# Kernel tuning notes

Measured on AMD Instinct MI355X. Metric: run time of the kernel, lower is better.

## Reference

```python
import jax, jax.numpy as jnp
import numpy as np

EPS = 1e-08


def setup_inputs() -> dict:
    key = jax.random.key(0)
    kx, km = jax.random.split(key)
    B, T, D = 128, 4096, 64
    x = jax.random.normal(kx, (B, T, D), dtype=jnp.float32)
    mask = jax.random.randint(km, (B, T, D), 0, 2).astype(jnp.float32)
    return {"x": x, "mask": mask}


def reference(x, mask):
    B, T, D = x.shape
    dt = x.dtype

    # ---- temporal: lag-1 autocorrelation + linear trend ----
    autocorr = jnp.mean(x[:, :-1, :] * x[:, 1:, :], axis=(1, 2))[:, None]  # (B,1)
    t = jnp.arange(T, dtype=dt)
    t_c = t - t.mean()
    x_mean_t = x.mean(axis=2)                                   # (B,T)
    num = (t_c * (x_mean_t - x_mean_t.mean(axis=1, keepdims=True))).sum(axis=1, keepdims=True)
    trend = num / ((t_c ** 2).sum() + EPS)                      # (B,1)

    # ---- frequency: dominant frequency + spectral entropy ----
    power = jnp.abs(jnp.fft.rfft(x_mean_t, axis=1)) ** 2        # (B,T//2+1)
    dom_freq = (jnp.argmax(power, axis=1).astype(dt) / (T / 2))[:, None]
    p_norm = power / (power.sum(axis=1, keepdims=True) + EPS)
    spec_ent = -(p_norm * jnp.log(p_norm + EPS)).sum(axis=1, keepdims=True)

    # ---- statistical: skewness, kurtosis, quantiles ----
    xc = x - x.mean(axis=(1, 2), keepdims=True)
    m2 = (xc ** 2).mean(axis=(1, 2))
    m3 = (xc ** 3).mean(axis=(1, 2))
    m4 = (xc ** 4).mean(axis=(1, 2))
    skew = m3 / (m2 ** 1.5 + EPS)
    kurt = m4 / (m2 ** 2 + EPS)
    q = jnp.quantile(x.reshape(B, -1), jnp.array([0.25, 0.5, 0.75]), axis=1)  # (3,B)
    stat = jnp.stack([skew, kurt, q[0], q[1], q[2]], axis=1)    # (B,5)

    # ---- shape: peaks, zero crossings, rate of change ----
    diff = x_mean_t[:, 1:] - x_mean_t[:, :-1]                   # (B,T-1)
    peak = (diff[:, 1:] * diff[:, :-1] < 0).astype(dt).sum(axis=1, keepdims=True) / (T - 2)
    xmc = x_mean_t - x_mean_t.mean(axis=1, keepdims=True)
    zero_cross = (xmc[:, 1:] * xmc[:, :-1] < 0).astype(dt).sum(axis=1, keepdims=True) / (T - 1)
    roc = jnp.abs(diff).mean(axis=1, keepdims=True)

    # ---- missing-data features (vectorized, no per-batch loop) ----
    missing_rate = 1.0 - mask.reshape(B, -1).sum(axis=1, keepdims=True) / (T * D + EPS)
    obs_per_time = mask.sum(axis=2)                             # (B,T)
    obs_density = obs_per_time / (D + EPS)
    density_var = jnp.var(obs_density, axis=1, ddof=1, keepdims=True)  # unbiased, matches torch
    time_mask = obs_per_time > 0                                # (B,T) bool
    first_idx = jnp.argmax(time_mask, axis=1).astype(dt)
    first_obs = jnp.where(time_mask.any(axis=1), first_idx / T, 0.0)[:, None]

    # ---- channel features: mean off-diagonal correlation + PCA var explained ----
    xcc = x - x.mean(axis=1, keepdims=True)                     # (B,T,D)
    gram = jnp.einsum('btd,bte->bde', xcc, xcc)                 # (B,D,D)
    cov = gram / (T - 1 + EPS)
    std = jnp.std(x, axis=1, ddof=1)                            # (B,D), unbiased like torch.std
    corr = cov / (std[:, :, None] * std[:, None, :] + EPS)
    off_diag = 1.0 - jnp.eye(D, dtype=dt)
    mean_corr = ((corr * off_diag).sum(axis=(1, 2)) / (D * (D - 1) + EPS))[:, None]
    # singular values squared of xcc == eigenvalues of gram
    eig = jnp.linalg.eigvalsh(gram)                             # ascending, (B,D)
    var_explained = (eig[:, -1] / eig.sum(axis=1))[:, None]

    return jnp.concatenate([
        autocorr, trend,               # temporal (2)
        dom_freq, spec_ent,            # frequency (2)
        stat,                          # statistical (5)
        peak, zero_cross, roc,         # shape (3)
        missing_rate, density_var, first_obs,  # missing (3)
        mean_corr, var_explained,      # channel (2)
    ], axis=1)                          # (B,17)
```

## Files before the change

kernel.cpp:

```cpp
#include <hip/hip_runtime.h>
#include <math.h>

#define TB 128
#define TT 4096
#define TD 64

#define GRAM_OFF   0u
#define HIST_OFF   2097152u
#define COLSUM_OFF 4194304u
#define SCAL_OFF   4227072u
#define FIRST_OFF  4230656u
#define ZERO_BYTES 4231168u
#define XMEAN_OFF  4231168u

typedef float  f32x4  __attribute__((ext_vector_type(4)));
typedef short  s16x8  __attribute__((ext_vector_type(8)));

__device__ __forceinline__ float brs4(float v, float* sbuf, int tid) {
#pragma unroll
  for (int o = 32; o; o >>= 1) v += __shfl_xor(v, o);
  __syncthreads();
  if ((tid & 63) == 0) sbuf[tid >> 6] = v;
  __syncthreads();
  return (sbuf[0] + sbuf[1]) + (sbuf[2] + sbuf[3]);
}

__device__ __forceinline__ float brs8(float v, float* sbuf, int tid) {
#pragma unroll
  for (int o = 32; o; o >>= 1) v += __shfl_xor(v, o);
  __syncthreads();
  if ((tid & 63) == 0) sbuf[tid >> 6] = v;
  __syncthreads();
  return ((sbuf[0] + sbuf[1]) + (sbuf[2] + sbuf[3])) +
         ((sbuf[4] + sbuf[5]) + (sbuf[6] + sbuf[7]));
}

__device__ __forceinline__ int binof(float v) {
  int bi = (int)floorf(fmaf(v, 256.f, 2048.f));
  return bi < 0 ? 0 : (bi > 4095 ? 4095 : bi);
}

__device__ __forceinline__ unsigned short f2bf(float f) {
  unsigned u = __float_as_uint(f);
  return (unsigned short)((u + 0x7FFFu + ((u >> 16) & 1u)) >> 16);
}

__global__ __launch_bounds__(256) void k1_fused(const float* __restrict__ x,
    const float* __restrict__ mk, float* __restrict__ xmean,
    float* __restrict__ gram, unsigned* __restrict__ hist,
    float* __restrict__ colsum, float* __restrict__ scal,
    int* __restrict__ firstg) {
  __shared__ __align__(16) float rows[64 * 72];
  __shared__ __align__(16) unsigned short Xt[64 * 72];
  __shared__ unsigned shist[4096];
  __shared__ float scol[64];
  __shared__ float sred[4];
  __shared__ int smax[4];

  const int tid  = threadIdx.x;
  const int b    = blockIdx.y;
  const int s    = blockIdx.x;
  const int t0   = s << 10;
  const int lane = tid & 63;
  const int wv   = tid >> 6;
  const int r0   = (tid >> 4) << 2;
  const int lcol = (tid & 15) << 2;
  const int rr   = tid >> 2;
  const int qq   = tid & 3;
  const int mb0 = (wv & 1) << 5;
  const int nb0 = (wv >> 1) << 5;
  const int ml  = lane & 15;
  const int qk  = (lane >> 4) << 3;

  for (int i = tid; i < 4096; i += 256) shist[i] = 0u;
  if (tid < 64) scol[tid] = 0.f;

  float s1 = 0.f, s2 = 0.f, s3 = 0.f, s4 = 0.f, ac = 0.f;
  float osum = 0.f, o2 = 0.f;
  int fmax = 0;
  float cs[4] = {0.f, 0.f, 0.f, 0.f};
  f32x4 acc[2][2];
#pragma unroll
  for (int mi = 0; mi < 2; ++mi)
#pragma unroll
    for (int ni = 0; ni < 2; ++ni) acc[mi][ni] = (f32x4)0.f;

  const float* xb = x + (size_t)b * (TT * TD);
  const float* mb = mk + (size_t)b * (TT * TD);

  __syncthreads();

  for (int tile = 0; tile < 16; ++tile) {
    const int tbase = t0 + (tile << 6);
    float4 v[4];
#pragma unroll
    for (int k = 0; k < 4; ++k) {
      const int r = r0 + k;
      v[k] = *(const float4*)(xb + (size_t)(tbase + r) * TD + lcol);
      const float x0 = v[k].x, x1 = v[k].y, x2 = v[k].z, x3 = v[k].w;
      const float q0 = x0 * x0, q1 = x1 * x1, q2 = x2 * x2, q3 = x3 * x3;
      s1 += (x0 + x1) + (x2 + x3);
      s2 += (q0 + q1) + (q2 + q3);
      s3 += (q0 * x0 + q1 * x1) + (q2 * x2 + q3 * x3);
      s4 += (q0 * q0 + q1 * q1) + (q2 * q2 + q3 * q3);
      cs[0] += x0; cs[1] += x1; cs[2] += x2; cs[3] += x3;
      atomicAdd(&shist[binof(x0)], 1u);
      atomicAdd(&shist[binof(x1)], 1u);
      atomicAdd(&shist[binof(x2)], 1u);
      atomicAdd(&shist[binof(x3)], 1u);
      *(float4*)(&rows[r * 72 + lcol]) = v[k];
    }
#pragma unroll
    for (int j = 0; j < 4; ++j) {
      const float e0 = j == 0 ? v[0].x : (j == 1 ? v[0].y : (j == 2 ? v[0].z : v[0].w));
      const float e1 = j == 0 ? v[1].x : (j == 1 ? v[1].y : (j == 2 ? v[1].z : v[1].w));
      const float e2 = j == 0 ? v[2].x : (j == 1 ? v[2].y : (j == 2 ? v[2].z : v[2].w));
      const float e3 = j == 0 ? v[3].x : (j == 1 ? v[3].y : (j == 2 ? v[3].z : v[3].w));
      uint2 pw;
      pw.x = (unsigned)f2bf(e0) | ((unsigned)f2bf(e1) << 16);
      pw.y = (unsigned)f2bf(e2) | ((unsigned)f2bf(e3) << 16);
      *(uint2*)(&Xt[(lcol + j) * 72 + r0]) = pw;
    }
#pragma unroll
    for (int k = 0; k < 4; ++k) {
      const int t = tbase + r0 + k;
      const float4 mv = *(const float4*)(mb + (size_t)t * TD + lcol);
      float ms = (mv.x + mv.y) + (mv.z + mv.w);
      ms += __shfl_xor(ms, 1);
      ms += __shfl_xor(ms, 2);
      ms += __shfl_xor(ms, 4);
      ms += __shfl_xor(ms, 8);
      if ((tid & 15) == 0) {
        osum += ms;
        o2 = fmaf(ms, ms, o2);
        if (ms > 0.f) fmax = max(fmax, TT - t);
      }
    }
    __syncthreads();
    {
      float4 c4[4];
      float rsum = 0.f;
#pragma unroll
      for (int j = 0; j < 4; ++j) {
        c4[j] = *(const float4*)(&rows[rr * 72 + (qq << 2) + (j << 4)]);
        rsum += (c4[j].x + c4[j].y) + (c4[j].z + c4[j].w);
      }
      float dot = 0.f;
      if (rr < 63) {
#pragma unroll
        for (int j = 0; j < 4; ++j) {
          const float4 n = *(const float4*)(&rows[(rr + 1) * 72 + (qq << 2) + (j << 4)]);
          dot += (c4[j].x * n.x + c4[j].y * n.y) + (c4[j].z * n.z + c4[j].w * n.w);
        }
      } else if (tbase + 64 < TT) {
        const float* np = xb + (size_t)(tbase + 64) * TD;
#pragma unroll
        for (int j = 0; j < 4; ++j) {
          const float4 n = *(const float4*)(np + (qq << 2) + (j << 4));
          dot += (c4[j].x * n.x + c4[j].y * n.y) + (c4[j].z * n.z + c4[j].w * n.w);
        }
      }
      ac += dot;
      rsum += __shfl_xor(rsum, 1);
      rsum += __shfl_xor(rsum, 2);
      if (qq == 0) xmean[(size_t)b * TT + tbase + rr] = rsum * (1.f / 64.f);
    }
#pragma unroll
    for (int kk = 0; kk < 2; ++kk) {
      const int ko = (kk << 5) + qk;
      s16x8 af[2], bf[2];
#pragma unroll
      for (int mi = 0; mi < 2; ++mi)
        af[mi] = *(const s16x8*)(&Xt[(mb0 + (mi << 4) + ml) * 72 + ko]);
#pragma unroll
      for (int ni = 0; ni < 2; ++ni)
        bf[ni] = *(const s16x8*)(&Xt[(nb0 + (ni << 4) + ml) * 72 + ko]);
#pragma unroll
      for (int mi = 0; mi < 2; ++mi)
#pragma unroll
        for (int ni = 0; ni < 2; ++ni)
          acc[mi][ni] = __builtin_amdgcn_mfma_f32_16x16x32_bf16(
              af[mi], bf[ni], acc[mi][ni], 0, 0, 0);
    }
    __syncthreads();
  }

  const float rac = brs4(ac, sred, tid);
  const float r1 = brs4(s1, sred, tid);
  const float r2 = brs4(s2, sred, tid);
  const float r3 = brs4(s3, sred, tid);
  const float r4 = brs4(s4, sred, tid);
  const float ro = brs4(osum, sred, tid);
  const float ro2 = brs4(o2, sred, tid);
#pragma unroll
  for (int o = 32; o; o >>= 1) fmax = max(fmax, __shfl_xor(fmax, o));
  if ((tid & 63) == 0) smax[tid >> 6] = fmax;
  __syncthreads();
  if (tid == 0) {
    atomicAdd(&scal[0 * TB + b], rac);
    atomicAdd(&scal[1 * TB + b], r1);
    atomicAdd(&scal[2 * TB + b], r2);
    atomicAdd(&scal[3 * TB + b], r3);
    atomicAdd(&scal[4 * TB + b], r4);
    atomicAdd(&scal[5 * TB + b], ro);
    atomicAdd(&scal[6 * TB + b], ro2);
    atomicMax(&firstg[b], max(max(smax[0], smax[1]), max(smax[2], smax[3])));
  }
#pragma unroll
  for (int c = 0; c < 4; ++c) atomicAdd(&scol[lcol + c], cs[c]);
  __syncthreads();
  if (tid < 64) atomicAdd(&colsum[b * 64 + tid], scol[tid]);
  float* gb = gram + (size_t)b * 4096;
  {
    const int crow = (lane >> 4) << 2;
    const int ccol = lane & 15;
#pragma unroll
    for (int mi = 0; mi < 2; ++mi)
#pragma unroll
      for (int ni = 0; ni < 2; ++ni) {
        const int gr0 = mb0 + (mi << 4) + crow;
        const int gc = nb0 + (ni << 4) + ccol;
#pragma unroll
        for (int rg = 0; rg < 4; ++rg)
          atomicAdd(&gb[(gr0 + rg) * 64 + gc], acc[mi][ni][rg]);
      }
  }
  unsigned* hb = hist + (size_t)b * 4096;
  for (int i = tid; i < 4096; i += 256) {
    const unsigned hv = shist[i];
    if (hv) atomicAdd(&hb[i], hv);
  }
}

__global__ __launch_bounds__(512) void k34(const float* __restrict__ xmean,
    const float* __restrict__ gram, const float* __restrict__ colsum,
    const unsigned* __restrict__ hist, const float* __restrict__ scal,
    const int* __restrict__ firstg, float* __restrict__ out) {
  __shared__ __align__(16) char arena[49152];
  __shared__ float sred[8];
  __shared__ float smv[8];
  __shared__ int smi[8];
  __shared__ float cssh[64];
  __shared__ float sdsh[64];
  __shared__ float osv_s[6];
  const int tid = threadIdx.x;

  if (blockIdx.x < 128) {
    const int b = blockIdx.x;
    float* xm = (float*)arena;
    float* re = xm + 4096;
    float* im = re + 4096;
    const float* xb = xmean + (size_t)b * TT;
    for (int i = tid; i < TT; i += 512) xm[i] = xb[i];
    __syncthreads();
    float ls = 0.f;
    for (int i = tid; i < TT; i += 512) ls += xm[i];
    const float meanv = brs8(ls, sred, tid) * (1.f / TT);
    float tnum = 0.f, roc = 0.f;
    int pk = 0, zc = 0;
    for (int i = tid; i < TT; i += 512) {
      const float xi = xm[i];
      tnum += ((float)i - 2047.5f) * (xi - meanv);
      if (i < TT - 1) {
        const float d1 = xm[i + 1] - xi;
        roc += fabsf(d1);
        if (i >= 1) {
          const float d0 = xi - xm[i - 1];
          if (d1 * d0 < 0.f) ++pk;
        }
      }
      if (i >= 1) {
        if ((xi - meanv) * (xm[i - 1] - meanv) < 0.f) ++zc;
      }
    }
    tnum = brs8(tnum, sred, tid);
    roc = brs8(roc, sred, tid);
    const float pkf = brs8((float)pk, sred, tid);
    const float zcf = brs8((float)zc, sred, tid);
    if (tid == 0) {
      out[b * 17 + 1] = tnum / 5726622720.0f;
      out[b * 17 + 9] = pkf * (1.f / 4094.f);
      out[b * 17 + 10] = zcf * (1.f / 4095.f);
      out[b * 17 + 11] = roc * (1.f / 4095.f);
    }
    for (int i = tid; i < TT; i += 512) {
      re[i] = xm[__brev((unsigned)i) >> 20];
      im[i] = 0.f;
    }
    __syncthreads();
    int l2h = 0;
    for (int len = 2; len <= TT; len <<= 1, ++l2h) {
      const int half = len >> 1;
      const float ab = -6.283185307179586f / (float)len;
      for (int j = tid; j < TT / 2; j += 512) {
        const int pos = j & (half - 1);
        const int i0 = ((j >> l2h) << (l2h + 1)) + pos;
        const int i1 = i0 + half;
        float sn, cn;
        __sincosf(ab * (float)pos, &sn, &cn);
        const float vr = re[i1], vi = im[i1];
        const float tr = cn * vr - sn * vi;
        const float ti = cn * vi + sn * vr;
        const float ur = re[i0], ui = im[i0];
        re[i0] = ur + tr; im[i0] = ui + ti;
        re[i1] = ur - tr; im[i1] = ui - ti;
      }
      __syncthreads();
    }
    float ps = 0.f, bmaxv = -1.f;
    int bidx = 0;
    for (int k = tid; k <= 2048; k += 512) {
      const float p = re[k] * re[k] + im[k] * im[k];
      ps += p;
      if (p > bmaxv) { bmaxv = p; bidx = k; }
    }
    ps = brs8(ps, sred, tid);
#pragma unroll
    for (int o = 32; o; o >>= 1) {
      const float ov = __shfl_xor(bmaxv, o);
      const int oi = __shfl_xor(bidx, o);
      if (ov > bmaxv || (ov == bmaxv && oi < bidx)) { bmaxv = ov; bidx = oi; }
    }
    if ((tid & 63) == 0) { smv[tid >> 6] = bmaxv; smi[tid >> 6] = bidx; }
    __syncthreads();
    float ent = 0.f;
    const float inv = 1.f / (ps + 1e-8f);
    for (int k = tid; k <= 2048; k += 512) {
      const float p = (re[k] * re[k] + im[k] * im[k]) * inv;
      ent -= p * __logf(p + 1e-8f);
    }
    ent = brs8(ent, sred, tid);
    if (tid == 0) {
      float bv = smv[0]; int bi = smi[0];
      for (int w = 1; w < 8; ++w)
        if (smv[w] > bv || (smv[w] == bv && smi[w] < bi)) { bv = smv[w]; bi = smi[w]; }
      out[b * 17 + 2] = (float)bi * (1.f / 2048.f);
      out[b * 17 + 3] = ent;
    }
  } else {
    const int b = blockIdx.x - 128;
    float* Lg = (float*)arena;
    unsigned* h = (unsigned*)(arena + 16640);
    unsigned* cumc = (unsigned*)(arena + 16640 + 16384);
    if (tid < 64) cssh[tid] = colsum[b * 64 + tid];
    for (int i = tid; i < 4096; i += 512) h[i] = hist[(size_t)b * 4096 + i];
    __syncthreads();
    const float* gb = gram + (size_t)b * 4096;
    for (int i = tid; i < 4096; i += 512) {
      const int d = i >> 6, e = i & 63;
      Lg[d * 65 + e] = gb[i] - cssh[d] * cssh[e] * (1.f / 4096.f);
    }
    unsigned chs_own = 0;
    if (tid < 256) {
#pragma unroll
      for (int j = 0; j < 16; ++j) chs_own += h[(tid << 4) + j];
      cumc[tid] = chs_own;
    }
    __syncthreads();
    if (tid < 64) sdsh[tid] = sqrtf(Lg[tid * 65 + tid] * (1.f / 4095.f));
    for (int off = 1; off < 256; off <<= 1) {
      unsigned add = 0;
      if (tid < 256 && tid >= off) add = cumc[tid - off];
      __syncthreads();
      if (tid < 256) cumc[tid] += add;
      __syncthreads();
    }
    float mcs = 0.f, trc = 0.f;
    for (int i = tid; i < 4096; i += 512) {
      const int d = i >> 6, e = i & 63;
      const float g = Lg[d * 65 + e];
      if (d != e) mcs += (g * (1.f / 4095.f)) / (sdsh[d] * sdsh[e] + 1e-8f);
      else trc += g;
    }
    mcs = brs8(mcs, sred, tid);
    trc = brs8(trc, sred, tid);
    if (tid < 256) {
      const unsigned ranks[6] = {65535u, 65536u, 131071u, 131072u, 196607u, 196608u};
      const unsigned incl = cumc[tid];
      const unsigned excl = incl - chs_own;
#pragma unroll
      for (int qi = 0; qi < 6; ++qi) {
        const unsigned r = ranks[qi];
        if (excl <= r && r < incl) {
          int bin = tid << 4;
          unsigned cum = excl;
          while (bin < 4095 && cum + h[bin] <= r) { cum += h[bin]; ++bin; }
          const float cnt = (float)max(h[bin], 1u);
          osv_s[qi] = ((float)bin * (1.f / 256.f) - 8.f) +
                      (((float)(r - cum) + 0.5f) / cnt) * (1.f / 256.f);
        }
      }
    }
    float lam = 0.f;
    if (tid < 64) {
      const float* rowp = &Lg[tid * 65];
      float v = 1.f + 0.001f * (float)tid;
      float n2 = 1.f;
      for (int it = 0; it < 48; ++it) {
        float w0 = 0.f, w1 = 0.f, w2 = 0.f, w3 = 0.f;
#pragma unroll
        for (int e = 0; e < 64; e += 4) {
          w0 = fmaf(rowp[e],     __shfl(v, e),     w0);
          w1 = fmaf(rowp[e + 1], __shfl(v, e + 1), w1);
          w2 = fmaf(rowp[e + 2], __shfl(v, e + 2), w2);
          w3 = fmaf(rowp[e + 3], __shfl(v, e + 3), w3);
        }
        const float w = (w0 + w1) + (w2 + w3);
        n2 = w * w;
#pragma unroll
        for (int o = 32; o; o >>= 1) n2 += __shfl_xor(n2, o);
        v = w * rsqrtf(n2);
      }
      lam = sqrtf(n2);
    }
    __syncthreads();
    if (tid == 0) {
      const float q25 = 0.25f * osv_s[0] + 0.75f * osv_s[1];
      const float q50 = 0.5f * (osv_s[2] + osv_s[3]);
      const float q75 = 0.75f * osv_s[4] + 0.25f * osv_s[5];
      const float N = 262144.f;
      const float m1 = scal[1 * TB + b] / N;
      const float M2 = scal[2 * TB + b] / N;
      const float M3 = scal[3 * TB + b] / N;
      const float M4 = scal[4 * TB + b] / N;
      const float mu2 = M2 - m1 * m1;
      const float mu3 = M3 - 3.f * m1 * M2 + 2.f * m1 * m1 * m1;
      const float mu4 = M4 - 4.f * m1 * M3 + 6.f * m1 * m1 * M2 - 3.f * m1 * m1 * m1 * m1;
      const float skew = mu3 / (sqrtf(mu2) * mu2 + 1e-8f);
      const float kurt = mu4 / (mu2 * mu2 + 1e-8f);
      const float acv = scal[0 * TB + b] * (1.f / 262080.f);
      const float msum = scal[5 * TB + b];
      const float o2s = scal[6 * TB + b];
      const float missing = 1.f - msum / 262144.f;
      const float sdm = msum * (1.f / 64.f) * (1.f / 4096.f);
      const float dvar = (o2s * (1.f / 4096.f) - 4096.f * sdm * sdm) * (1.f / 4095.f);
      const int fm = firstg[b];
      const float fobs = fm > 0 ? (float)(4096 - fm) * (1.f / 4096.f) : 0.f;
      float* ob = out + b * 17;
      ob[0] = acv;
      ob[4] = skew; ob[5] = kurt;
      ob[6] = q25; ob[7] = q50; ob[8] = q75;
      ob[12] = missing; ob[13] = dvar; ob[14] = fobs;
      ob[15] = mcs / (4032.f + 1e-8f);
      ob[16] = lam / trc;
    }
  }
}

extern "C" void kernel_launch(void* const* d_in, const int* in_sizes, int n_in,
                              void* d_out, int out_size, void* d_ws, size_t ws_size,
                              hipStream_t stream) {
  (void)in_sizes; (void)n_in; (void)out_size; (void)ws_size;
  const float* x = (const float*)d_in[0];
  const float* mask = (const float*)d_in[1];
  float* out = (float*)d_out;
  char* ws = (char*)d_ws;
  float* gram = (float*)(ws + GRAM_OFF);
  unsigned* hist = (unsigned*)(ws + HIST_OFF);
  float* colsum = (float*)(ws + COLSUM_OFF);
  float* scal = (float*)(ws + SCAL_OFF);
  int* firstg = (int*)(ws + FIRST_OFF);
  float* xmean = (float*)(ws + XMEAN_OFF);

  hipMemsetAsync(d_ws, 0, ZERO_BYTES, stream);

  dim3 g1(4, TB);
  k1_fused<<<g1, 256, 0, stream>>>(x, mask, xmean, gram, hist, colsum, scal, firstg);
  k34<<<256, 512, 0, stream>>>(xmean, gram, colsum, hist, scal, firstg, out);
}
```

Before: 360.1 us.

## Double-buffer tiles with register prefetch and compute row stats in registers

Restructures the fused main kernel so the next tile's x and mask loads are prefetched into registers while MFMA and the statistics for the current tile run. The bf16 transpose buffer is double-buffered, which leaves one barrier per tile instead of two. The fp32 rows buffer is removed: row means and the lag-1 products are computed from registers with shuffles, and a small boundary buffer supplies the neighbouring row across thread groups. The grid doubles to 8 blocks per batch over half as many tiles each, raising parallelism at the cost of more global atomics to gram, hist and scalars.

After: 406.3 us. 1.13x slower.

```diff
diff --git a/kernel.cpp b/kernel.cpp
--- a/kernel.cpp
+++ b/kernel.cpp
@@ -50,9 +50,9 @@
     float* __restrict__ gram, unsigned* __restrict__ hist,
     float* __restrict__ colsum, float* __restrict__ scal,
     int* __restrict__ firstg) {
-  __shared__ __align__(16) float rows[64 * 72];
-  __shared__ __align__(16) unsigned short Xt[64 * 72];
+  __shared__ __align__(16) unsigned short Xt[2][64 * 72];
   __shared__ unsigned shist[4096];
+  __shared__ float bnd[2][4][64];
   __shared__ float scol[64];
   __shared__ float sred[4];
   __shared__ int smax[4];
@@ -60,13 +60,13 @@
   const int tid  = threadIdx.x;
   const int b    = blockIdx.y;
   const int s    = blockIdx.x;
-  const int t0   = s << 10;
+  const int t0   = s << 9;
   const int lane = tid & 63;
   const int wv   = tid >> 6;
-  const int r0   = (tid >> 4) << 2;
-  const int lcol = (tid & 15) << 2;
-  const int rr   = tid >> 2;
-  const int qq   = tid & 3;
+  const int g    = tid >> 4;
+  const int r0   = g << 2;
+  const int c    = tid & 15;
+  const int lcol = c << 2;
   const int mb0 = (wv & 1) << 5;
   const int nb0 = (wv >> 1) << 5;
   const int ml  = lane & 15;
@@ -86,17 +86,56 @@
     for (int ni = 0; ni < 2; ++ni) acc[mi][ni] = (f32x4)0.f;
 
   const float* xb = x + (size_t)b * (TT * TD);
-  const float* mb = mk + (size_t)b * (TT * TD);
-
-  __syncthreads();
-
-  for (int tile = 0; tile < 16; ++tile) {
+  const float* mbp = mk + (size_t)b * (TT * TD);
+
+  float4 v[4], mv[4];
+#pragma unroll
+  for (int k = 0; k < 4; ++k) {
+    v[k]  = *(const float4*)(xb  + (size_t)(t0 + r0 + k) * TD + lcol);
+    mv[k] = *(const float4*)(mbp + (size_t)(t0 + r0 + k) * TD + lcol);
+  }
+
+  int p = 0;
+  for (int tile = 0; tile < 8; ++tile) {
     const int tbase = t0 + (tile << 6);
-    float4 v[4];
+#pragma unroll
+    for (int j = 0; j < 4; ++j) {
+      const int jj = (j + c + g) & 3;
+      uint2 pw;
+      pw.x = (unsigned)f2bf((&v[0].x)[jj]) | ((unsigned)f2bf((&v[1].x)[jj]) << 16);
+      pw.y = (unsigned)f2bf((&v[2].x)[jj]) | ((unsigned)f2bf((&v[3].x)[jj]) << 16);
+      *(uint2*)(&Xt[p][(lcol + jj) * 72 + r0]) = pw;
+    }
+    if ((g & 3) == 0) *(float4*)(&bnd[p][g >> 2][lcol]) = v[0];
+    __syncthreads();
+    float4 vn[4], mn[4];
+    if (tile < 7) {
+      const int tn = tbase + 64;
+#pragma unroll
+      for (int k = 0; k < 4; ++k) {
+        vn[k] = *(const float4*)(xb  + (size_t)(tn + r0 + k) * TD + lcol);
+        mn[k] = *(const float4*)(mbp + (size_t)(tn + r0 + k) * TD + lcol);
+      }
+    }
+#pragma unroll
+    for (int kk = 0; kk < 2; ++kk) {
+      const int ko = (kk << 5) + qk;
+      s16x8 af[2], bf[2];
+#pragma unroll
+      for (int mi = 0; mi < 2; ++mi)
+        af[mi] = *(const s16x8*)(&Xt[p][(mb0 + (mi << 4) + ml) * 72 + ko]);
+#pragma unroll
+      for (int ni = 0; ni < 2; ++ni)
+        bf[ni] = *(const s16x8*)(&Xt[p][(nb0 + (ni << 4) + ml) * 72 + ko]);
+#pragma unroll
+      for (int mi = 0; mi < 2; ++mi)
+#pragma unroll
+        for (int ni = 0; ni < 2; ++ni)
+          acc[mi][ni] = __builtin_amdgcn_mfma_f32_16x16x32_bf16(
+              af[mi], bf[ni], acc[mi][ni], 0, 0, 0);
+    }
 #pragma unroll
     for (int k = 0; k < 4; ++k) {
-      const int r = r0 + k;
-      v[k] = *(const float4*)(xb + (size_t)(tbase + r) * TD + lcol);
       const float x0 = v[k].x, x1 = v[k].y, x2 = v[k].z, x3 = v[k].w;
       const float q0 = x0 * x0, q1 = x1 * x1, q2 = x2 * x2, q3 = x3 * x3;
       s1 += (x0 + x1) + (x2 + x3);
@@ -108,81 +147,48 @@
       atomicAdd(&shist[binof(x1)], 1u);
       atomicAdd(&shist[binof(x2)], 1u);
       atomicAdd(&shist[binof(x3)], 1u);
-      *(float4*)(&rows[r * 72 + lcol]) = v[k];
-    }
-#pragma unroll
-    for (int j = 0; j < 4; ++j) {
-      const float e0 = j == 0 ? v[0].x : (j == 1 ? v[0].y : (j == 2 ? v[0].z : v[0].w));
-      const float e1 = j == 0 ? v[1].x : (j == 1 ? v[1].y : (j == 2 ? v[1].z : v[1].w));
-      const float e2 = j == 0 ? v[2].x : (j == 1 ? v[2].y : (j == 2 ? v[2].z : v[2].w));
-      const float e3 = j == 0 ? v[3].x : (j == 1 ? v[3].y : (j == 2 ? v[3].z : v[3].w));
-      uint2 pw;
-      pw.x = (unsigned)f2bf(e0) | ((unsigned)f2bf(e1) << 16);
-      pw.y = (unsigned)f2bf(e2) | ((unsigned)f2bf(e3) << 16);
-      *(uint2*)(&Xt[(lcol + j) * 72 + r0]) = pw;
     }
 #pragma unroll
     for (int k = 0; k < 4; ++k) {
-      const int t = tbase + r0 + k;
-      const float4 mv = *(const float4*)(mb + (size_t)t * TD + lcol);
-      float ms = (mv.x + mv.y) + (mv.z + mv.w);
-      ms += __shfl_xor(ms, 1);
-      ms += __shfl_xor(ms, 2);
-      ms += __shfl_xor(ms, 4);
-      ms += __shfl_xor(ms, 8);
-      if ((tid & 15) == 0) {
-        osum += ms;
-        o2 = fmaf(ms, ms, o2);
-        if (ms > 0.f) fmax = max(fmax, TT - t);
-      }
-    }
-    __syncthreads();
+      float rx = (v[k].x + v[k].y) + (v[k].z + v[k].w);
+      float rm = (mv[k].x + mv[k].y) + (mv[k].z + mv[k].w);
+      rx += __shfl_xor(rx, 1); rm += __shfl_xor(rm, 1);
+      rx += __shfl_xor(rx, 2); rm += __shfl_xor(rm, 2);
+      rx += __shfl_xor(rx, 4); rm += __shfl_xor(rm, 4);
+      rx += __shfl_xor(rx, 8); rm += __shfl_xor(rm, 8);
+      if (c == 0) {
+        const int t = tbase + r0 + k;
+        xmean[(size_t)b * TT + t] = rx * (1.f / 64.f);
+        osum += rm;
+        o2 = fmaf(rm, rm, o2);
+        if (rm > 0.f) fmax = max(fmax, TT - t);
+      }
+    }
     {
-      float4 c4[4];
-      float rsum = 0.f;
-#pragma unroll
-      for (int j = 0; j < 4; ++j) {
-        c4[j] = *(const float4*)(&rows[rr * 72 + (qq << 2) + (j << 4)]);
-        rsum += (c4[j].x + c4[j].y) + (c4[j].z + c4[j].w);
-      }
-      float dot = 0.f;
-      if (rr < 63) {
-#pragma unroll
-        for (int j = 0; j < 4; ++j) {
-          const float4 n = *(const float4*)(&rows[(rr + 1) * 72 + (qq << 2) + (j << 4)]);
-          dot += (c4[j].x * n.x + c4[j].y * n.y) + (c4[j].z * n.z + c4[j].w * n.w);
+      float dot =
+          (v[0].x * v[1].x + v[0].y * v[1].y) + (v[0].z * v[1].z + v[0].w * v[1].w) +
+          (v[1].x * v[2].x + v[1].y * v[2].y) + (v[1].z * v[2].z + v[1].w * v[2].w) +
+          (v[2].x * v[3].x + v[2].y * v[3].y) + (v[2].z * v[3].z + v[2].w * v[3].w);
+      if ((g & 3) == 3) {
+        float4 nx;
+        bool have = true;
+        if (g < 15) {
+          nx = *(const float4*)(&bnd[p][(g >> 2) + 1][lcol]);
+        } else if (tbase + 64 < TT) {
+          nx = *(const float4*)(xb + (size_t)(tbase + 64) * TD + lcol);
+        } else {
+          have = false;
         }
-      } else if (tbase + 64 < TT) {
-        const float* np = xb + (size_t)(tbase + 64) * TD;
-#pragma unroll
-        for (int j = 0; j < 4; ++j) {
-          const float4 n = *(const float4*)(np + (qq << 2) + (j << 4));
-          dot += (c4[j].x * n.x + c4[j].y * n.y) + (c4[j].z * n.z + c4[j].w * n.w);
-        }
+        if (have)
+          dot += (v[3].x * nx.x + v[3].y * nx.y) + (v[3].z * nx.z + v[3].w * nx.w);
       }
       ac += dot;
-      rsum += __shfl_xor(rsum, 1);
-      rsum += __shfl_xor(rsum, 2);
-      if (qq == 0) xmean[(size_t)b * TT + tbase + rr] = rsum * (1.f / 64.f);
-    }
-#pragma unroll
-    for (int kk = 0; kk < 2; ++kk) {
-      const int ko = (kk << 5) + qk;
-      s16x8 af[2], bf[2];
-#pragma unroll
-      for (int mi = 0; mi < 2; ++mi)
-        af[mi] = *(const s16x8*)(&Xt[(mb0 + (mi << 4) + ml) * 72 + ko]);
-#pragma unroll
-      for (int ni = 0; ni < 2; ++ni)
-        bf[ni] = *(const s16x8*)(&Xt[(nb0 + (ni << 4) + ml) * 72 + ko]);
-#pragma unroll
-      for (int mi = 0; mi < 2; ++mi)
-#pragma unroll
-        for (int ni = 0; ni < 2; ++ni)
-          acc[mi][ni] = __builtin_amdgcn_mfma_f32_16x16x32_bf16(
-              af[mi], bf[ni], acc[mi][ni], 0, 0, 0);
-    }
-    __syncthreads();
+    }
+    if (tile < 7) {
+#pragma unroll
+      for (int k = 0; k < 4; ++k) { v[k] = vn[k]; mv[k] = mn[k]; }
+    }
+    p ^= 1;
   }
 
   const float rac = brs4(ac, sred, tid);
@@ -207,7 +213,7 @@
     atomicMax(&firstg[b], max(max(smax[0], smax[1]), max(smax[2], smax[3])));
   }
 #pragma unroll
-  for (int c = 0; c < 4; ++c) atomicAdd(&scol[lcol + c], cs[c]);
+  for (int cc = 0; cc < 4; ++cc) atomicAdd(&scol[lcol + cc], cs[cc]);
   __syncthreads();
   if (tid < 64) atomicAdd(&colsum[b * 64 + tid], scol[tid]);
   float* gb = gram + (size_t)b * 4096;
@@ -368,9 +374,9 @@
     float mcs = 0.f, trc = 0.f;
     for (int i = tid; i < 4096; i += 512) {
       const int d = i >> 6, e = i & 63;
-      const float g = Lg[d * 65 + e];
-      if (d != e) mcs += (g * (1.f / 4095.f)) / (sdsh[d] * sdsh[e] + 1e-8f);
-      else trc += g;
+      const float gv = Lg[d * 65 + e];
+      if (d != e) mcs += (gv * (1.f / 4095.f)) / (sdsh[d] * sdsh[e] + 1e-8f);
+      else trc += gv;
     }
     mcs = brs8(mcs, sred, tid);
     trc = brs8(trc, sred, tid);
@@ -464,7 +470,7 @@
 
   hipMemsetAsync(d_ws, 0, ZERO_BYTES, stream);
 
-  dim3 g1(4, TB);
+  dim3 g1(8, TB);
   k1_fused<<<g1, 256, 0, stream>>>(x, mask, xmean, gram, hist, colsum, scal, firstg);
   k34<<<256, 512, 0, stream>>>(xmean, gram, colsum, hist, scal, firstg, out);
 }
```
